# Performance work log

Hardware: AMD Instinct MI355X
Metric: run time of the kernel (lower is better)

## Reference

```python
import jax, jax.numpy as jnp
import numpy as np

N = 65536          # number of atoms (routing tokens)
NUM_SPECIES = 4    # number of per-species expert models
D_IN, D_HID, D_OUT = 256, 1024, 256


def setup_inputs() -> dict:
    key = jax.random.key(0)
    k = jax.random.split(key, 6)
    x = jax.random.normal(k[0], (N, D_IN), dtype=jnp.float32)
    central_species = jax.random.randint(k[1], (N,), 0, NUM_SPECIES, dtype=jnp.int64)
    # Per-species 2-layer MLP experts, stacked along species axis.
    W1 = jax.random.normal(k[2], (NUM_SPECIES, D_IN, D_HID), dtype=jnp.float32) * (1.0 / np.sqrt(D_IN))
    b1 = jnp.zeros((NUM_SPECIES, D_HID), dtype=jnp.float32)
    W2 = jax.random.normal(k[3], (NUM_SPECIES, D_HID, D_OUT), dtype=jnp.float32) * (1.0 / np.sqrt(D_HID))
    b2 = jnp.zeros((NUM_SPECIES, D_OUT), dtype=jnp.float32)
    return {"x": x, "central_species": central_species, "W1": W1, "b1": b1, "W2": W2, "b2": b2}


def reference(x, central_species, W1, b1, W2, b2):
    # Equivalent to: split rows by species (CentralSplitter), apply the
    # species-specific submodel, scatter results back by mask (CentralUniter).
    # Dense-compute-and-select expression: every row receives exactly the
    # output of its own species' expert, identical math to masked gather/scatter.
    num_species = W1.shape[0]
    out = jnp.zeros((x.shape[0], W2.shape[-1]), dtype=x.dtype)
    for s in range(num_species):  # small fixed expert count
        h = jax.nn.silu(x @ W1[s] + b1[s])          # [N, D_HID]
        y = h @ W2[s] + b2[s]                       # [N, D_OUT]
        sel = (central_species == s)[:, None]
        out = out + jnp.where(sel, y, jnp.zeros_like(y))
    return out
```

## Files before the change

### kernel.cpp

```cpp
#include <hip/hip_runtime.h>
#include <hip/hip_bf16.h>


#define N_ATOMS 65536
#define D_IN 256
#define D_HID 1024
#define D_OUT 256
#define TPS 1024

typedef __attribute__((ext_vector_type(8))) short short8;
typedef __attribute__((ext_vector_type(4))) float float4e;

#define WS_BUCKET_OFF 256
#define WS_W1_OFF 1048832
#define WS_W2_OFF 3145984

__device__ __forceinline__ short f2bf(float f) {
  unsigned u = __builtin_bit_cast(unsigned, f);
  unsigned r = (u + 0x7FFFu + ((u >> 16) & 1u)) >> 16;
  return (short)r;
}

__global__ void prep_kernel(const float* __restrict__ W1, const float* __restrict__ W2,
                            short* __restrict__ w1sw, short* __restrict__ w2sw,
                            int* __restrict__ cnt) {
  int gid = blockIdx.x * 256 + threadIdx.x;
  if (gid < 64) cnt[gid] = 0;
  int lane = gid & 63;
  int lr = lane & 15;
  int lk = (lane >> 4) * 8;
  if (gid < 131072) {
    int ks = (gid >> 6) & 7;
    int nt = (gid >> 9) & 63;
    int s  = gid >> 15;
    const float* src = W1 + ((size_t)(s * 256 + ks * 32 + lk)) * 1024 + nt * 16 + lr;
    short8 v;
    for (int j = 0; j < 8; ++j) v[j] = f2bf(src[(size_t)j * 1024]);
    *(short8*)(w1sw + (size_t)gid * 8) = v;
  } else {
    int g = gid - 131072;
    int kt = (g >> 6) & 31;
    int nt = (g >> 11) & 15;
    int s  = g >> 15;
    const float* src = W2 + ((size_t)(s * 1024 + kt * 32 + lk)) * 256 + nt * 16 + lr;
    short8 v;
    for (int j = 0; j < 8; ++j) v[j] = f2bf(src[(size_t)j * 256]);
    *(short8*)(w2sw + (size_t)g * 8) = v;
  }
}

__global__ void count_fill_kernel(const int* __restrict__ species,
                                  int* __restrict__ cnt, int* __restrict__ bucket) {
  int tid = threadIdx.x;
  int i = blockIdx.x * 256 + tid;
  int s = species[i] & 3;
  int lane = tid & 63, wid = tid >> 6;
  __shared__ int wcnt[4][4];
  __shared__ int wbase[4][4];
  unsigned long long m0 = __ballot(s == 0);
  unsigned long long m1 = __ballot(s == 1);
  unsigned long long m2 = __ballot(s == 2);
  unsigned long long m3 = __ballot(s == 3);
  if (lane == 0) {
    wcnt[wid][0] = __popcll(m0); wcnt[wid][1] = __popcll(m1);
    wcnt[wid][2] = __popcll(m2); wcnt[wid][3] = __popcll(m3);
  }
  __syncthreads();
  if (tid < 4) {
    int ss = tid;
    int c0 = wcnt[0][ss], c1 = wcnt[1][ss], c2 = wcnt[2][ss], c3 = wcnt[3][ss];
    int base = atomicAdd(&cnt[ss * 16], c0 + c1 + c2 + c3);
    wbase[0][ss] = base;
    wbase[1][ss] = base + c0;
    wbase[2][ss] = base + c0 + c1;
    wbase[3][ss] = base + c0 + c1 + c2;
  }
  __syncthreads();
  unsigned long long below = (1ull << lane) - 1ull;
  int rank = 0;
  if (s == 0) rank = __popcll(m0 & below);
  if (s == 1) rank = __popcll(m1 & below);
  if (s == 2) rank = __popcll(m2 & below);
  if (s == 3) rank = __popcll(m3 & below);
  bucket[s * N_ATOMS + wbase[wid][s] + rank] = i;
}

#define XS_STRIDE 280
#define HS_STRIDE 152
__global__ __launch_bounds__(256, 2) void fused_kernel(
    const float* __restrict__ x, const int* __restrict__ cntArr,
    const int* __restrict__ bucket, const short* __restrict__ w1sw,
    const short* __restrict__ w2sw, const float* __restrict__ b1,
    const float* __restrict__ b2, float* __restrict__ out) {
  int s = blockIdx.x >> 10;
  int t = blockIdx.x & (TPS - 1);
  int cnt = cntArr[s * 16];
  int r0 = t * 64;
  if (r0 >= cnt) return;
  int nrows = min(64, cnt - r0);
  const int* buck = bucket + s * N_ATOMS + r0;

  __shared__ short Xs[64 * XS_STRIDE];
  __shared__ short Hs[2][64 * HS_STRIDE];

  int tid = threadIdx.x;

  for (int i = 0; i < 8; ++i) {
    int id = tid + i * 256;
    int r = id >> 5;
    int g = id & 31;
    short8 v = {};
    if (r < nrows) {
      const float4* src = (const float4*)(x + (size_t)buck[r] * D_IN + g * 8);
      float4 f0 = src[0];
      float4 f1 = src[1];
      v[0] = f2bf(f0.x); v[1] = f2bf(f0.y); v[2] = f2bf(f0.z); v[3] = f2bf(f0.w);
      v[4] = f2bf(f1.x); v[5] = f2bf(f1.y); v[6] = f2bf(f1.z); v[7] = f2bf(f1.w);
    }
    *(short8*)(Xs + r * XS_STRIDE + g * 8) = v;
  }

  int lane = tid & 63;
  int wid = tid >> 6;
  int lr = lane & 15;
  int lk = (lane >> 4) * 8;
  int lq = (lane >> 4) * 4;

  float bias1[8][2];
  #pragma unroll
  for (int c = 0; c < 8; ++c)
    #pragma unroll
    for (int ct = 0; ct < 2; ++ct)
      bias1[c][ct] = b1[s * D_HID + c * 128 + wid * 32 + ct * 16 + lr];
  float bias2[4];
  #pragma unroll
  for (int ct = 0; ct < 4; ++ct)
    bias2[ct] = b2[s * D_OUT + wid * 64 + ct * 16 + lr];

  short8 b1f[16];
  #pragma unroll
  for (int ks = 0; ks < 8; ++ks)
    #pragma unroll
    for (int ct = 0; ct < 2; ++ct) {
      int nt = 0 * 8 + wid * 2 + ct;
      b1f[ks * 2 + ct] = *(const short8*)(w1sw + ((size_t)((s * 64 + nt) * 8 + ks)) * 512 + lane * 8);
    }

  __syncthreads();

  float4e accY[4][4] = {};

  for (int c = 0; c < 8; ++c) {
    float4e acc1[4][2] = {};
    #pragma unroll
    for (int ks = 0; ks < 8; ++ks) {
      short8 a[4];
      #pragma unroll
      for (int rt = 0; rt < 4; ++rt)
        a[rt] = *(const short8*)(Xs + (rt * 16 + lr) * XS_STRIDE + ks * 32 + lk);
      #pragma unroll
      for (int rt = 0; rt < 4; ++rt)
        #pragma unroll
        for (int ct = 0; ct < 2; ++ct)
          acc1[rt][ct] = __builtin_amdgcn_mfma_f32_16x16x32_bf16(a[rt], b1f[ks * 2 + ct], acc1[rt][ct], 0, 0, 0);
    }
    short8 b2f[16];
    #pragma unroll
    for (int ks = 0; ks < 4; ++ks)
      #pragma unroll
      for (int ct = 0; ct < 4; ++ct) {
        int nt = wid * 4 + ct;
        int kt = c * 4 + ks;
        b2f[ks * 4 + ct] = *(const short8*)(w2sw + ((size_t)((s * 16 + nt) * 32 + kt)) * 512 + lane * 8);
      }
    short* hsb = Hs[c & 1];
    #pragma unroll
    for (int ct = 0; ct < 2; ++ct) {
      int nloc = wid * 32 + ct * 16 + lr;
      float bias = bias1[c][ct];
      #pragma unroll
      for (int rt = 0; rt < 4; ++rt) {
        float4e v4 = acc1[rt][ct];
        #pragma unroll
        for (int q = 0; q < 4; ++q) {
          float pre = v4[q] + bias;
          float val = pre / (1.0f + __expf(-pre));
          hsb[(rt * 16 + lq + q) * HS_STRIDE + nloc] = f2bf(val);
        }
      }
    }
    __syncthreads();
    if (c < 7) {
      #pragma unroll
      for (int ks = 0; ks < 8; ++ks)
        #pragma unroll
        for (int ct = 0; ct < 2; ++ct) {
          int nt = (c + 1) * 8 + wid * 2 + ct;
          b1f[ks * 2 + ct] = *(const short8*)(w1sw + ((size_t)((s * 64 + nt) * 8 + ks)) * 512 + lane * 8);
        }
    }
    #pragma unroll
    for (int ks = 0; ks < 4; ++ks) {
      short8 a[4];
      #pragma unroll
      for (int rt = 0; rt < 4; ++rt)
        a[rt] = *(const short8*)(hsb + (rt * 16 + lr) * HS_STRIDE + ks * 32 + lk);
      #pragma unroll
      for (int rt = 0; rt < 4; ++rt)
        #pragma unroll
        for (int ct = 0; ct < 4; ++ct)
          accY[rt][ct] = __builtin_amdgcn_mfma_f32_16x16x32_bf16(a[rt], b2f[ks * 4 + ct], accY[rt][ct], 0, 0, 0);
    }
  }

  #pragma unroll
  for (int ct = 0; ct < 4; ++ct) {
    int n = wid * 64 + ct * 16 + lr;
    float bias = bias2[ct];
    #pragma unroll
    for (int rt = 0; rt < 4; ++rt) {
      #pragma unroll
      for (int q = 0; q < 4; ++q) {
        int r = rt * 16 + lq + q;
        if (r < nrows)
          out[(size_t)buck[r] * D_OUT + n] = accY[rt][ct][q] + bias;
      }
    }
  }
}

extern "C" void kernel_launch(void* const* d_in, const int* in_sizes, int n_in,
                              void* d_out, int out_size, void* d_ws, size_t ws_size,
                              hipStream_t stream) {
  const float* x  = (const float*)d_in[0];
  const int* spc  = (const int*)d_in[1];
  const float* W1 = (const float*)d_in[2];
  const float* b1 = (const float*)d_in[3];
  const float* W2 = (const float*)d_in[4];
  const float* b2 = (const float*)d_in[5];
  float* out = (float*)d_out;

  int*   cnt    = (int*)d_ws;
  int*   bucket = (int*)((char*)d_ws + WS_BUCKET_OFF);
  short* w1sw   = (short*)((char*)d_ws + WS_W1_OFF);
  short* w2sw   = (short*)((char*)d_ws + WS_W2_OFF);

  prep_kernel<<<1024, 256, 0, stream>>>(W1, W2, w1sw, w2sw, cnt);
  count_fill_kernel<<<N_ATOMS / 256, 256, 0, stream>>>(spc, cnt, bucket);
  fused_kernel<<<4 * TPS, 256, 0, stream>>>(x, cnt, bucket, w1sw, w2sw, b1, b2, out);
}
```

Baseline: 257.9 us.

## Transpose MFMA operands for vectorized stores, batch bucketing, interleave species blocks

Swaps the MFMA operand order so weights form the A operand and activations the B operand. Each lane then holds four contiguous output columns, which allows short4 stores of the hidden activations to LDS and float4 stores of the outputs to global memory. Biases are folded into the accumulator initial values, and the SiLU division becomes a reciprocal multiply. Bucket filling now runs in 32 blocks of 8 iterations, with one atomic per species per block. Blocks for different species are interleaved so early-exiting blocks are spread out, at the cost of more complex index arithmetic.

```diff
diff --git a/kernel.cpp b/kernel.cpp
--- a/kernel.cpp
+++ b/kernel.cpp
@@ -9,6 +9,7 @@
 #define TPS 1024
 
 typedef __attribute__((ext_vector_type(8))) short short8;
+typedef __attribute__((ext_vector_type(4))) short short4v;
 typedef __attribute__((ext_vector_type(4))) float float4e;
 
 #define WS_BUCKET_OFF 256
@@ -49,40 +50,51 @@
   }
 }
 
+#define CF_BLOCKS 32
+#define CF_ITERS 8
 __global__ void count_fill_kernel(const int* __restrict__ species,
                                   int* __restrict__ cnt, int* __restrict__ bucket) {
   int tid = threadIdx.x;
-  int i = blockIdx.x * 256 + tid;
-  int s = species[i] & 3;
   int lane = tid & 63, wid = tid >> 6;
-  __shared__ int wcnt[4][4];
-  __shared__ int wbase[4][4];
-  unsigned long long m0 = __ballot(s == 0);
-  unsigned long long m1 = __ballot(s == 1);
-  unsigned long long m2 = __ballot(s == 2);
-  unsigned long long m3 = __ballot(s == 3);
-  if (lane == 0) {
-    wcnt[wid][0] = __popcll(m0); wcnt[wid][1] = __popcll(m1);
-    wcnt[wid][2] = __popcll(m2); wcnt[wid][3] = __popcll(m3);
+  __shared__ int wcnt[CF_ITERS][4][4];
+  __shared__ int wb[CF_ITERS][4][4];
+  __shared__ int base_sm[4];
+  int sv[CF_ITERS], rk[CF_ITERS];
+  unsigned long long below = (1ull << lane) - 1ull;
+  int base_i = blockIdx.x * (CF_ITERS * 256);
+  #pragma unroll
+  for (int it = 0; it < CF_ITERS; ++it) {
+    int s = species[base_i + it * 256 + tid] & 3;
+    sv[it] = s;
+    unsigned long long m0 = __ballot(s == 0);
+    unsigned long long m1 = __ballot(s == 1);
+    unsigned long long m2 = __ballot(s == 2);
+    unsigned long long m3 = __ballot(s == 3);
+    unsigned long long ms = (s == 0) ? m0 : (s == 1) ? m1 : (s == 2) ? m2 : m3;
+    rk[it] = __popcll(ms & below);
+    if (lane == 0) {
+      wcnt[it][wid][0] = __popcll(m0);
+      wcnt[it][wid][1] = __popcll(m1);
+      wcnt[it][wid][2] = __popcll(m2);
+      wcnt[it][wid][3] = __popcll(m3);
+    }
   }
   __syncthreads();
   if (tid < 4) {
-    int ss = tid;
-    int c0 = wcnt[0][ss], c1 = wcnt[1][ss], c2 = wcnt[2][ss], c3 = wcnt[3][ss];
-    int base = atomicAdd(&cnt[ss * 16], c0 + c1 + c2 + c3);
-    wbase[0][ss] = base;
-    wbase[1][ss] = base + c0;
-    wbase[2][ss] = base + c0 + c1;
-    wbase[3][ss] = base + c0 + c1 + c2;
+    int ss = tid, run = 0;
+    for (int it = 0; it < CF_ITERS; ++it)
+      for (int w = 0; w < 4; ++w) {
+        wb[it][w][ss] = run;
+        run += wcnt[it][w][ss];
+      }
+    base_sm[ss] = atomicAdd(&cnt[ss * 16], run);
   }
   __syncthreads();
-  unsigned long long below = (1ull << lane) - 1ull;
-  int rank = 0;
-  if (s == 0) rank = __popcll(m0 & below);
-  if (s == 1) rank = __popcll(m1 & below);
-  if (s == 2) rank = __popcll(m2 & below);
-  if (s == 3) rank = __popcll(m3 & below);
-  bucket[s * N_ATOMS + wbase[wid][s] + rank] = i;
+  #pragma unroll
+  for (int it = 0; it < CF_ITERS; ++it) {
+    int ss = sv[it];
+    bucket[ss * N_ATOMS + base_sm[ss] + wb[it][wid][ss] + rk[it]] = base_i + it * 256 + tid;
+  }
 }
 
 #define XS_STRIDE 280
@@ -92,8 +104,9 @@
     const int* __restrict__ bucket, const short* __restrict__ w1sw,
     const short* __restrict__ w2sw, const float* __restrict__ b1,
     const float* __restrict__ b2, float* __restrict__ out) {
-  int s = blockIdx.x >> 10;
-  int t = blockIdx.x & (TPS - 1);
+  int bid = blockIdx.x;
+  int s = (bid & 7) >> 1;
+  int t = ((bid >> 3) << 1) | (bid & 1);
   int cnt = cntArr[s * 16];
   int r0 = t * 64;
   if (r0 >= cnt) return;
@@ -126,67 +139,76 @@
   int lk = (lane >> 4) * 8;
   int lq = (lane >> 4) * 4;
 
-  float bias1[8][2];
-  #pragma unroll
-  for (int c = 0; c < 8; ++c)
-    #pragma unroll
-    for (int ct = 0; ct < 2; ++ct)
-      bias1[c][ct] = b1[s * D_HID + c * 128 + wid * 32 + ct * 16 + lr];
-  float bias2[4];
-  #pragma unroll
-  for (int ct = 0; ct < 4; ++ct)
-    bias2[ct] = b2[s * D_OUT + wid * 64 + ct * 16 + lr];
+  int rowIdx[4];
+  #pragma unroll
+  for (int bt = 0; bt < 4; ++bt) {
+    int r = bt * 16 + lr;
+    rowIdx[bt] = (r < nrows) ? buck[r] : -1;
+  }
+
+  float4e accY[4][4];
+  #pragma unroll
+  for (int at = 0; at < 4; ++at) {
+    float4e bv = *(const float4e*)(b2 + s * D_OUT + wid * 64 + at * 16 + lq);
+    #pragma unroll
+    for (int bt = 0; bt < 4; ++bt) accY[at][bt] = bv;
+  }
 
   short8 b1f[16];
   #pragma unroll
   for (int ks = 0; ks < 8; ++ks)
     #pragma unroll
-    for (int ct = 0; ct < 2; ++ct) {
-      int nt = 0 * 8 + wid * 2 + ct;
-      b1f[ks * 2 + ct] = *(const short8*)(w1sw + ((size_t)((s * 64 + nt) * 8 + ks)) * 512 + lane * 8);
+    for (int at = 0; at < 2; ++at) {
+      int nt = 0 * 8 + wid * 2 + at;
+      b1f[ks * 2 + at] = *(const short8*)(w1sw + ((size_t)((s * 64 + nt) * 8 + ks)) * 512 + lane * 8);
     }
 
   __syncthreads();
 
-  float4e accY[4][4] = {};
-
   for (int c = 0; c < 8; ++c) {
-    float4e acc1[4][2] = {};
+    float4e acc1[2][4];
+    #pragma unroll
+    for (int at = 0; at < 2; ++at) {
+      float4e bv = *(const float4e*)(b1 + s * D_HID + c * 128 + wid * 32 + at * 16 + lq);
+      #pragma unroll
+      for (int bt = 0; bt < 4; ++bt) acc1[at][bt] = bv;
+    }
     #pragma unroll
     for (int ks = 0; ks < 8; ++ks) {
-      short8 a[4];
-      #pragma unroll
-      for (int rt = 0; rt < 4; ++rt)
-        a[rt] = *(const short8*)(Xs + (rt * 16 + lr) * XS_STRIDE + ks * 32 + lk);
-      #pragma unroll
-      for (int rt = 0; rt < 4; ++rt)
-        #pragma unroll
-        for (int ct = 0; ct < 2; ++ct)
-          acc1[rt][ct] = __builtin_amdgcn_mfma_f32_16x16x32_bf16(a[rt], b1f[ks * 2 + ct], acc1[rt][ct], 0, 0, 0);
+      short8 xb[4];
+      #pragma unroll
+      for (int bt = 0; bt < 4; ++bt)
+        xb[bt] = *(const short8*)(Xs + (bt * 16 + lr) * XS_STRIDE + ks * 32 + lk);
+      #pragma unroll
+      for (int at = 0; at < 2; ++at)
+        #pragma unroll
+        for (int bt = 0; bt < 4; ++bt)
+          acc1[at][bt] = __builtin_amdgcn_mfma_f32_16x16x32_bf16(b1f[ks * 2 + at], xb[bt], acc1[at][bt], 0, 0, 0);
     }
     short8 b2f[16];
     #pragma unroll
     for (int ks = 0; ks < 4; ++ks)
       #pragma unroll
-      for (int ct = 0; ct < 4; ++ct) {
-        int nt = wid * 4 + ct;
+      for (int at = 0; at < 4; ++at) {
+        int nt = wid * 4 + at;
         int kt = c * 4 + ks;
-        b2f[ks * 4 + ct] = *(const short8*)(w2sw + ((size_t)((s * 16 + nt) * 32 + kt)) * 512 + lane * 8);
+        b2f[ks * 4 + at] = *(const short8*)(w2sw + ((size_t)((s * 16 + nt) * 32 + kt)) * 512 + lane * 8);
       }
     short* hsb = Hs[c & 1];
     #pragma unroll
-    for (int ct = 0; ct < 2; ++ct) {
-      int nloc = wid * 32 + ct * 16 + lr;
-      float bias = bias1[c][ct];
-      #pragma unroll
-      for (int rt = 0; rt < 4; ++rt) {
-        float4e v4 = acc1[rt][ct];
+    for (int at = 0; at < 2; ++at) {
+      int hidloc = wid * 32 + at * 16 + lq;
+      #pragma unroll
+      for (int bt = 0; bt < 4; ++bt) {
+        float4e v4 = acc1[at][bt];
+        short4v hv;
         #pragma unroll
         for (int q = 0; q < 4; ++q) {
-          float pre = v4[q] + bias;
-          float val = pre / (1.0f + __expf(-pre));
-          hsb[(rt * 16 + lq + q) * HS_STRIDE + nloc] = f2bf(val);
+          float pre = v4[q];
+          float val = pre * __builtin_amdgcn_rcpf(1.0f + __expf(-pre));
+          hv[q] = f2bf(val);
         }
+        *(short4v*)(hsb + (bt * 16 + lr) * HS_STRIDE + hidloc) = hv;
       }
     }
     __syncthreads();
@@ -194,37 +216,32 @@
       #pragma unroll
       for (int ks = 0; ks < 8; ++ks)
         #pragma unroll
-        for (int ct = 0; ct < 2; ++ct) {
-          int nt = (c + 1) * 8 + wid * 2 + ct;
-          b1f[ks * 2 + ct] = *(const short8*)(w1sw + ((size_t)((s * 64 + nt) * 8 + ks)) * 512 + lane * 8);
+        for (int at = 0; at < 2; ++at) {
+          int nt = (c + 1) * 8 + wid * 2 + at;
+          b1f[ks * 2 + at] = *(const short8*)(w1sw + ((size_t)((s * 64 + nt) * 8 + ks)) * 512 + lane * 8);
         }
     }
     #pragma unroll
     for (int ks = 0; ks < 4; ++ks) {
-      short8 a[4];
-      #pragma unroll
-      for (int rt = 0; rt < 4; ++rt)
-        a[rt] = *(const short8*)(hsb + (rt * 16 + lr) * HS_STRIDE + ks * 32 + lk);
-      #pragma unroll
-      for (int rt = 0; rt < 4; ++rt)
-        #pragma unroll
-        for (int ct = 0; ct < 4; ++ct)
-          accY[rt][ct] = __builtin_amdgcn_mfma_f32_16x16x32_bf16(a[rt], b2f[ks * 4 + ct], accY[rt][ct], 0, 0, 0);
-    }
-  }
-
-  #pragma unroll
-  for (int ct = 0; ct < 4; ++ct) {
-    int n = wid * 64 + ct * 16 + lr;
-    float bias = bias2[ct];
-    #pragma unroll
-    for (int rt = 0; rt < 4; ++rt) {
-      #pragma unroll
-      for (int q = 0; q < 4; ++q) {
-        int r = rt * 16 + lq + q;
-        if (r < nrows)
-          out[(size_t)buck[r] * D_OUT + n] = accY[rt][ct][q] + bias;
-      }
+      short8 hb[4];
+      #pragma unroll
+      for (int bt = 0; bt < 4; ++bt)
+        hb[bt] = *(const short8*)(hsb + (bt * 16 + lr) * HS_STRIDE + ks * 32 + lk);
+      #pragma unroll
+      for (int at = 0; at < 4; ++at)
+        #pragma unroll
+        for (int bt = 0; bt < 4; ++bt)
+          accY[at][bt] = __builtin_amdgcn_mfma_f32_16x16x32_bf16(b2f[ks * 4 + at], hb[bt], accY[at][bt], 0, 0, 0);
+    }
+  }
+
+  #pragma unroll
+  for (int at = 0; at < 4; ++at) {
+    int nb = wid * 64 + at * 16 + lq;
+    #pragma unroll
+    for (int bt = 0; bt < 4; ++bt) {
+      if (rowIdx[bt] >= 0)
+        *(float4e*)(out + (size_t)rowIdx[bt] * D_OUT + nb) = accY[at][bt];
     }
   }
 }
@@ -246,6 +263,6 @@
   short* w2sw   = (short*)((char*)d_ws + WS_W2_OFF);
 
   prep_kernel<<<1024, 256, 0, stream>>>(W1, W2, w1sw, w2sw, cnt);
-  count_fill_kernel<<<N_ATOMS / 256, 256, 0, stream>>>(spc, cnt, bucket);
+  count_fill_kernel<<<CF_BLOCKS, 256, 0, stream>>>(spc, cnt, bucket);
   fused_kernel<<<4 * TPS, 256, 0, stream>>>(x, cnt, bucket, w1sw, w2sw, b1, b2, out);
 }
```

After: 226.2 us. 12.3% less time.
